# Optimization experiments

Measured on AMD Instinct MI355X. Metric: run time of the kernel, lower is better.

Reference implementation:

```python
import jax, jax.numpy as jnp
import numpy as np

HEADS = 16
DIM_HEAD = 64

def setup_inputs() -> dict:
    key = jax.random.key(0)
    ks = jax.random.split(key, 7)
    B, Nq, Dq = 4, 2048, 1024
    Nk, Dc = 1024, 768
    inner = HEADS * DIM_HEAD  # 1024
    sq = 1.0 / np.sqrt(Dq)
    sc = 1.0 / np.sqrt(Dc)
    si = 1.0 / np.sqrt(inner)
    return {
        "x": jax.random.normal(ks[0], (B, Nq, Dq), dtype=jnp.float32),
        "context": jax.random.normal(ks[1], (B, Nk, Dc), dtype=jnp.float32),
        "Wq": jax.random.normal(ks[2], (Dq, inner), dtype=jnp.float32) * sq,
        "Wk": jax.random.normal(ks[3], (Dc, inner), dtype=jnp.float32) * sc,
        "Wv": jax.random.normal(ks[4], (Dc, inner), dtype=jnp.float32) * sc,
        "Wo": jax.random.normal(ks[5], (inner, Dq), dtype=jnp.float32) * si,
        "bo": jax.random.normal(ks[6], (Dq,), dtype=jnp.float32) * 0.01,
    }

def reference(x, context, Wq, Wk, Wv, Wo, bo):
    B, Nq, _ = x.shape
    Nk = context.shape[1]
    h, dh = HEADS, DIM_HEAD
    # projections (no bias on q/k/v, matching nn.Linear(bias=False))
    q = (x @ Wq).reshape(B, Nq, h, dh)        # [B,Nq,h,dh]
    k = (context @ Wk).reshape(B, Nk, h, dh)  # [B,Nk,h,dh]
    v = (context @ Wv).reshape(B, Nk, h, dh)
    scale = 1.0 / jnp.sqrt(jnp.asarray(dh, dtype=x.dtype))
    # scores: [B,h,Nq,Nk]
    scores = jnp.einsum('bqhd,bkhd->bhqk', q, k) * scale
    attn = jax.nn.softmax(scores, axis=-1)
    out = jnp.einsum('bhqk,bkhd->bqhd', attn, v).reshape(B, Nq, h * dh)
    return out @ Wo + bo
```

## Files before the change

kernel.cpp:

```cpp
#include <hip/hip_runtime.h>

typedef __bf16 bf16;
typedef __bf16 bf16x2 __attribute__((ext_vector_type(2)));
typedef __bf16 bf16x4 __attribute__((ext_vector_type(4)));
typedef __bf16 bf16x8 __attribute__((ext_vector_type(8)));
typedef float f32x4 __attribute__((ext_vector_type(4)));

#define MFMA(a, b, c) __builtin_amdgcn_mfma_f32_16x16x32_bf16(a, b, c, 0, 0, 0)

#define GLD16(gptr, ldsptr)                                                        \
  __builtin_amdgcn_global_load_lds(                                                \
      (const __attribute__((address_space(1))) unsigned int*)(gptr),               \
      (__attribute__((address_space(3))) unsigned int*)(ldsptr), 16, 0, 0)

union I4B8 { int4 i; bf16x8 v; };
union HI { bf16x2 h; int i; };

__global__ __launch_bounds__(256) void prep_k(const float* __restrict__ x, bf16* __restrict__ xb,
                                              const float* __restrict__ ctx, bf16* __restrict__ ctxb,
                                              const float* __restrict__ Wq, bf16* __restrict__ WqT,
                                              const float* __restrict__ Wk, bf16* __restrict__ WkvT,
                                              const float* __restrict__ Wv,
                                              const float* __restrict__ Wo, bf16* __restrict__ WoT) {
  __shared__ float t[32][33];
  const int bid = blockIdx.x;
  if (bid < 5632) {
    const float* in; bf16* out; size_t i;
    if (bid < 4096) { in = x; out = xb; i = ((size_t)bid * 256 + threadIdx.x) * 8; }
    else { in = ctx; out = ctxb; i = ((size_t)(bid - 4096) * 256 + threadIdx.x) * 8; }
    const float4 a = *(const float4*)(in + i);
    const float4 b = *(const float4*)(in + i + 4);
    bf16x8 o;
    o[0] = (bf16)a.x; o[1] = (bf16)a.y; o[2] = (bf16)a.z; o[3] = (bf16)a.w;
    o[4] = (bf16)b.x; o[5] = (bf16)b.y; o[6] = (bf16)b.z; o[7] = (bf16)b.w;
    *(bf16x8*)(out + i) = o;
    return;
  }
  const int tt = bid - 5632;
  const int z = tt >> 10, rem = tt & 1023;
  const float* in; bf16* out; int R; float sc = 1.0f;
  if (z == 0)      { in = Wq; out = WqT;                R = 1024; sc = 0.18033688f; }
  else if (z == 1) { in = Wk; out = WkvT;               R = 768; }
  else if (z == 2) { in = Wv; out = WkvT + 1024 * 768;  R = 768; }
  else             { in = Wo; out = WoT;                R = 1024; }
  const int c0 = (rem & 31) * 32, r0 = (rem >> 5) * 32;
  if (r0 >= R) return;
  const int tx = threadIdx.x & 31, ty = threadIdx.x >> 5;
#pragma unroll
  for (int i = 0; i < 4; i++)
    t[ty + i * 8][tx] = in[(size_t)(r0 + ty + i * 8) * 1024 + c0 + tx];
  __syncthreads();
#pragma unroll
  for (int i = 0; i < 4; i++)
    out[(size_t)(c0 + ty + i * 8) * R + r0 + tx] = (bf16)(t[tx][ty + i * 8] * sc);
}

template <int MODE>
__device__ __forceinline__ void phase_mma(const bf16* Ls, int Abase, int Bbase,
                                          int wm, int wn, int q, int c, int swz,
                                          f32x4 (&pacc)[4][2]) {
  bf16x8 af[4][2], bb[2][2];
#pragma unroll
  for (int mi = 0; mi < 4; mi++) {
    const int rr = wm * 64 + mi * 16 + c;
#pragma unroll
    for (int kk = 0; kk < 2; kk++)
      af[mi][kk] = *(const bf16x8*)&Ls[Abase + rr * 64 + ((kk * 32 + q * 8) ^ swz)];
  }
#pragma unroll
  for (int ni = 0; ni < 2; ni++) {
    const int rn = wn * 32 + ni * 16 + c;
#pragma unroll
    for (int kk = 0; kk < 2; kk++)
      bb[ni][kk] = *(const bf16x8*)&Ls[Bbase + rn * 64 + ((kk * 32 + q * 8) ^ swz)];
  }
  __builtin_amdgcn_s_setprio(1);
#pragma unroll
  for (int mi = 0; mi < 4; mi++)
#pragma unroll
    for (int ni = 0; ni < 2; ni++)
#pragma unroll
      for (int kk = 0; kk < 2; kk++) {
        if constexpr (MODE == 2)
          pacc[mi][ni] = MFMA(af[mi][kk], bb[ni][kk], pacc[mi][ni]);
        else
          pacc[mi][ni] = MFMA(bb[ni][kk], af[mi][kk], pacc[mi][ni]);
      }
  __builtin_amdgcn_s_setprio(0);
}

template <int MODE>
__device__ __forceinline__ void gemm256(const bf16* __restrict__ A,
                                        const bf16* __restrict__ Bt,
                                        int K, int m0, int n0,
                                        void* __restrict__ C0,
                                        bf16* Ls) {
  const int tid = threadIdx.x;
  const int lane = tid & 63, w = tid >> 6;
  const int wm = w >> 2, wn = w & 3;
  const int q = lane >> 4, c = lane & 15;
  const int swz = (c & 7) * 8;

  const int rl = tid >> 3, seg = tid & 7;
  const bf16* Ag = A + (size_t)(m0 + rl) * K + ((seg ^ (rl & 7)) * 8);
  const bf16* Bg = Bt + (size_t)(n0 + rl) * K + ((seg ^ (rl & 7)) * 8);
  const size_t K64 = (size_t)K * 64, K128 = (size_t)K * 128;
  const int ws = w * 512;

  f32x4 acc[2][2][4][2] = {};

  GLD16(Ag,              &Ls[0 + ws]);
  GLD16(Ag + K64,        &Ls[4096 + ws]);
  GLD16(Ag + K128,       &Ls[8192 + ws]);
  GLD16(Ag + K128 + K64, &Ls[8192 + 4096 + ws]);
  GLD16(Bg,              &Ls[32768 + ws]);
  GLD16(Bg + K64,        &Ls[32768 + 4096 + ws]);
  GLD16(Bg + K128,       &Ls[32768 + 8192 + ws]);
  GLD16(Bg + K128 + K64, &Ls[32768 + 8192 + 4096 + ws]);

  int cur = 0;
  for (int k0 = 0; k0 < K; k0 += 64) {
    const int nxt = cur ^ 1;
    const size_t kn = (size_t)((k0 + 64 < K) ? k0 + 64 : k0);
    const int Ab = cur * 16384, Bb = 32768 + cur * 16384;
    const int An = nxt * 16384, Bn = 32768 + nxt * 16384;

    asm volatile("s_waitcnt vmcnt(2)" ::: "memory");
    asm volatile("s_barrier" ::: "memory");
    GLD16(Ag + kn,       &Ls[An + ws]);
    GLD16(Ag + kn + K64, &Ls[An + 4096 + ws]);
    phase_mma<MODE>(Ls, Ab, Bb, wm, wn, q, c, swz, acc[0][0]);

    asm volatile("s_waitcnt vmcnt(2)" ::: "memory");
    asm volatile("s_barrier" ::: "memory");
    GLD16(Ag + kn + K128,       &Ls[An + 8192 + ws]);
    GLD16(Ag + kn + K128 + K64, &Ls[An + 8192 + 4096 + ws]);
    phase_mma<MODE>(Ls, Ab, Bb + 8192, wm, wn, q, c, swz, acc[0][1]);

    asm volatile("s_barrier" ::: "memory");
    GLD16(Bg + kn,       &Ls[Bn + ws]);
    GLD16(Bg + kn + K64, &Ls[Bn + 4096 + ws]);
    phase_mma<MODE>(Ls, Ab + 8192, Bb, wm, wn, q, c, swz, acc[1][0]);

    asm volatile("s_barrier" ::: "memory");
    GLD16(Bg + kn + K128,       &Ls[Bn + 8192 + ws]);
    GLD16(Bg + kn + K128 + K64, &Ls[Bn + 8192 + 4096 + ws]);
    phase_mma<MODE>(Ls, Ab + 8192, Bb + 8192, wm, wn, q, c, swz, acc[1][1]);

    cur = nxt;
  }
  asm volatile("s_waitcnt vmcnt(0)" ::: "memory");

  if constexpr (MODE == 0) {
#pragma unroll
    for (int h = 0; h < 2; h++)
#pragma unroll
      for (int g = 0; g < 2; g++)
#pragma unroll
        for (int ni = 0; ni < 2; ni++) {
          const int col = n0 + g * 128 + wn * 32 + ni * 16 + q * 4;
#pragma unroll
          for (int mi = 0; mi < 4; mi++) {
            const int row = m0 + h * 128 + wm * 64 + mi * 16 + c;
            bf16x4 vv;
#pragma unroll
            for (int r2 = 0; r2 < 4; r2++) vv[r2] = (bf16)acc[h][g][mi][ni][r2];
            *(bf16x4*)&((bf16*)C0)[(size_t)row * 1024 + col] = vv;
          }
        }
  } else {
#pragma unroll
    for (int h = 0; h < 2; h++)
#pragma unroll
      for (int g = 0; g < 2; g++)
#pragma unroll
        for (int ni = 0; ni < 2; ni++) {
          const int col = n0 + g * 128 + wn * 32 + ni * 16 + c;
#pragma unroll
          for (int mi = 0; mi < 4; mi++) {
            const int rbase = m0 + h * 128 + wm * 64 + mi * 16 + q * 4;
            const int b = rbase >> 10, key = rbase & 1023;
            bf16* VT = (bf16*)C0;
            const int hh = col >> 6, d = col & 63;
            const int kl = key & 63;
            const int pkey = (key & ~63) | (kl & 32) | ((kl & 12) << 1) | ((kl & 16) >> 2);
            bf16x4 vv;
#pragma unroll
            for (int r2 = 0; r2 < 4; r2++) vv[r2] = (bf16)acc[h][g][mi][ni][r2];
            *(bf16x4*)&VT[((size_t)(b * 16 + hh) * 64 + d) * 1024 + pkey] = vv;
          }
        }
  }
}

__global__ __launch_bounds__(512) void proj_k(const bf16* __restrict__ xb,
                                              const bf16* __restrict__ ctxb,
                                              const bf16* __restrict__ WqT,
                                              const bf16* __restrict__ WkvT,
                                              bf16* __restrict__ Q,
                                              bf16* __restrict__ Kp,
                                              bf16* __restrict__ VT) {
  extern __shared__ __align__(16) bf16 Ls[];
  const int bid = blockIdx.x;
  if (bid < 128) {
    const int x = bid & 7, i = bid >> 3;
    const int rt = x * 4 + (i >> 2), ct = i & 3;
    gemm256<0>(xb, WqT, 1024, rt * 256, ct * 256, Q, Ls);
  } else if (bid < 192) {
    const int t = bid - 128, x = t & 7, i = t >> 3;
    const int rt = x * 2 + (i >> 2), ct = i & 3;
    gemm256<0>(ctxb, WkvT, 768, rt * 256, ct * 256, Kp, Ls);
  } else {
    const int t = bid - 192, x = t & 7, i = t >> 3;
    const int rt = x * 2 + (i >> 2), ct = i & 3;
    gemm256<2>(ctxb, WkvT + (size_t)1024 * 768, 768, rt * 256, ct * 256, VT, Ls);
  }
}

template <int MODE>
__device__ __forceinline__ void gemm_body(const bf16* __restrict__ A,
                                          const bf16* __restrict__ Bt,
                                          int K, int m0, int n0,
                                          void* __restrict__ C0,
                                          const float* __restrict__ bias,
                                          bf16* As, bf16* Bs) {
  const int tid = threadIdx.x;
  const int lane = tid & 63, wave = tid >> 6;
  const int wm = wave >> 1, wn = wave & 1;
  const int q = lane >> 4, c = lane & 15;

  f32x4 acc[4][4] = {};
  const int r = tid >> 3;
  const int col8 = ((tid & 7) * 8) ^ ((r & 7) * 8);
  const bf16* Ag = A + (size_t)(m0 + r) * K + col8;
  const bf16* Bg = Bt + (size_t)(n0 + r) * K + col8;
  const size_t K32 = (size_t)K * 32;
  bf16* AsW = As + wave * 512;
  bf16* BsW = Bs + wave * 512;
  const int swz = (c & 7) * 8;

  for (int k0 = 0; k0 < K; k0 += 64) {
    __syncthreads();
    GLD16(Ag + k0,            AsW);
    GLD16(Ag + k0 + K32,      AsW + 2048);
    GLD16(Ag + k0 + 2 * K32,  AsW + 4096);
    GLD16(Ag + k0 + 3 * K32,  AsW + 6144);
    GLD16(Bg + k0,            BsW);
    GLD16(Bg + k0 + K32,      BsW + 2048);
    GLD16(Bg + k0 + 2 * K32,  BsW + 4096);
    GLD16(Bg + k0 + 3 * K32,  BsW + 6144);
    __syncthreads();
#pragma unroll
    for (int kk = 0; kk < 2; kk++) {
      const int cx = (kk * 32 + q * 8) ^ swz;
      bf16x8 af[4], bfr[4];
#pragma unroll
      for (int mi = 0; mi < 4; mi++)
        af[mi] = *(const bf16x8*)&As[(wm * 64 + mi * 16 + c) * 64 + cx];
#pragma unroll
      for (int ni = 0; ni < 4; ni++)
        bfr[ni] = *(const bf16x8*)&Bs[(wn * 64 + ni * 16 + c) * 64 + cx];
      __builtin_amdgcn_s_setprio(1);
#pragma unroll
      for (int mi = 0; mi < 4; mi++)
#pragma unroll
        for (int ni = 0; ni < 4; ni++)
          acc[mi][ni] = MFMA(bfr[ni], af[mi], acc[mi][ni]);
      __builtin_amdgcn_s_setprio(0);
    }
  }

#pragma unroll
  for (int ni = 0; ni < 4; ni++) {
    const int col = n0 + wn * 64 + ni * 16 + q * 4;
    float4 bv4 = *(const float4*)&bias[col];
#pragma unroll
    for (int mi = 0; mi < 4; mi++) {
      const int row = m0 + wm * 64 + mi * 16 + c;
      f32x4 vv;
      vv[0] = acc[mi][ni][0] + bv4.x; vv[1] = acc[mi][ni][1] + bv4.y;
      vv[2] = acc[mi][ni][2] + bv4.z; vv[3] = acc[mi][ni][3] + bv4.w;
      *(f32x4*)&((float*)C0)[(size_t)row * 1024 + col] = vv;
    }
  }
}

__global__ __launch_bounds__(256) void out_k(const bf16* __restrict__ O,
                                             const bf16* __restrict__ WoT,
                                             float* __restrict__ out,
                                             const float* __restrict__ bo) {
  __shared__ __align__(16) bf16 As[8192];
  __shared__ __align__(16) bf16 Bs[8192];
  const int bid = blockIdx.x;
  const int s = (bid & 7) * 64 + (bid >> 3);
  gemm_body<1>(O, WoT, 1024, (s >> 3) * 128, (s & 7) * 128, out, bo, As, Bs);
}

__global__ __launch_bounds__(256, 2) void attn_k(const bf16* __restrict__ Qg,
                                                 const bf16* __restrict__ Kg,
                                                 const bf16* __restrict__ VTg,
                                                 bf16* __restrict__ Og) {
  __shared__ __align__(16) bf16 Ks[64][72];
  __shared__ __align__(16) bf16 Vt[64][72];
  const int tid = threadIdx.x;
  const int lane = tid & 63, w = tid >> 6;
  const int q = lane >> 4, c = lane & 15;
  const int bid = blockIdx.x;
  const int pair = (bid & 7) * 8 + (bid >> 6);
  const int head = pair & 15, b = pair >> 4;
  const int q0 = ((bid >> 3) & 7) * 256;

  bf16x8 aQ[4][2];
#pragma unroll
  for (int mj = 0; mj < 4; mj++)
#pragma unroll
    for (int ks = 0; ks < 2; ks++)
      aQ[mj][ks] = *(const bf16x8*)(Qg + (size_t)(b * 2048 + q0 + w * 64 + mj * 16 + c) * 1024 +
                                    head * 64 + ks * 32 + q * 8);

  f32x4 o[4][4] = {};
  f32x4 ol[4] = {};
  bf16x8 vone;
#pragma unroll
  for (int i = 0; i < 8; i++) vone[i] = (bf16)1.0f;

  const int srow = tid >> 2, sc = tid & 3;
  const bf16* Kbase = Kg + (size_t)(b * 1024 + srow) * 1024 + head * 64 + sc * 16;
  const bf16* Vbase = VTg + ((size_t)(b * 16 + head) * 64 + srow) * 1024 + sc * 16;

  bf16x8 rk0 = *(const bf16x8*)(Kbase);
  bf16x8 rk1 = *(const bf16x8*)(Kbase + 8);
  bf16x8 rv0 = *(const bf16x8*)(Vbase);
  bf16x8 rv1 = *(const bf16x8*)(Vbase + 8);

  for (int kt = 0; kt < 16; kt++) {
    __syncthreads();
    *(bf16x8*)&Ks[srow][sc * 16]     = rk0;
    *(bf16x8*)&Ks[srow][sc * 16 + 8] = rk1;
    *(bf16x8*)&Vt[srow][sc * 16]     = rv0;
    *(bf16x8*)&Vt[srow][sc * 16 + 8] = rv1;
    if (kt < 15) {
      const size_t ko = (size_t)(kt + 1) * 64 * 1024;
      const int vo = (kt + 1) * 64;
      rk0 = *(const bf16x8*)(Kbase + ko);
      rk1 = *(const bf16x8*)(Kbase + ko + 8);
      rv0 = *(const bf16x8*)(Vbase + vo);
      rv1 = *(const bf16x8*)(Vbase + vo + 8);
    }
    __syncthreads();

    f32x4 st[4][4] = {};
#pragma unroll
    for (int ks = 0; ks < 2; ks++) {
      bf16x8 ak[4];
#pragma unroll
      for (int ni = 0; ni < 4; ni++) ak[ni] = *(const bf16x8*)&Ks[ni * 16 + c][ks * 32 + q * 8];
      __builtin_amdgcn_s_setprio(1);
#pragma unroll
      for (int mj = 0; mj < 4; mj++)
#pragma unroll
        for (int ni = 0; ni < 4; ni++)
          st[mj][ni] = MFMA(ak[ni], aQ[mj][ks], st[mj][ni]);
      __builtin_amdgcn_s_setprio(0);
    }

    int pk[4][4][2];
#pragma unroll
    for (int mj = 0; mj < 4; mj++)
#pragma unroll
      for (int ni = 0; ni < 4; ni++) {
        float p0 = __builtin_amdgcn_exp2f(st[mj][ni][0]);
        float p1 = __builtin_amdgcn_exp2f(st[mj][ni][1]);
        float p2 = __builtin_amdgcn_exp2f(st[mj][ni][2]);
        float p3 = __builtin_amdgcn_exp2f(st[mj][ni][3]);
        HI h0, h1;
        h0.h[0] = (bf16)p0; h0.h[1] = (bf16)p1;
        h1.h[0] = (bf16)p2; h1.h[1] = (bf16)p3;
        pk[mj][ni][0] = h0.i;
        pk[mj][ni][1] = h1.i;
      }

#pragma unroll
    for (int ks2 = 0; ks2 < 2; ks2++) {
      bf16x8 bv[4];
#pragma unroll
      for (int ni = 0; ni < 4; ni++)
        bv[ni] = *(const bf16x8*)&Vt[ni * 16 + c][ks2 * 32 + q * 8];
#pragma unroll
      for (int mi = 0; mi < 4; mi++) {
        I4B8 pa;
        pa.i.x = pk[mi][2 * ks2][0];
        pa.i.y = pk[mi][2 * ks2][1];
        pa.i.z = pk[mi][2 * ks2 + 1][0];
        pa.i.w = pk[mi][2 * ks2 + 1][1];
        __builtin_amdgcn_s_setprio(1);
#pragma unroll
        for (int ni = 0; ni < 4; ni++)
          o[mi][ni] = MFMA(pa.v, bv[ni], o[mi][ni]);
        ol[mi] = MFMA(pa.v, vone, ol[mi]);
        __builtin_amdgcn_s_setprio(0);
      }
    }
  }

#pragma unroll
  for (int mi = 0; mi < 4; mi++) {
    float inv[4];
#pragma unroll
    for (int r = 0; r < 4; r++) inv[r] = 1.0f / ol[mi][r];
#pragma unroll
    for (int ni = 0; ni < 4; ni++)
#pragma unroll
      for (int r = 0; r < 4; r++) {
        const int qrow = q0 + w * 64 + mi * 16 + q * 4 + r;
        const int col = head * 64 + ni * 16 + c;
        Og[(size_t)(b * 2048 + qrow) * 1024 + col] = (bf16)(o[mi][ni][r] * inv[r]);
      }
  }
}

extern "C" void kernel_launch(void* const* d_in, const int* in_sizes, int n_in,
                              void* d_out, int out_size, void* d_ws, size_t ws_size,
                              hipStream_t stream) {
  (void)in_sizes; (void)n_in; (void)out_size; (void)ws_size;
  const float* x   = (const float*)d_in[0];
  const float* ctx = (const float*)d_in[1];
  const float* Wq  = (const float*)d_in[2];
  const float* Wk  = (const float*)d_in[3];
  const float* Wv  = (const float*)d_in[4];
  const float* Wo  = (const float*)d_in[5];
  const float* bo  = (const float*)d_in[6];
  float* out = (float*)d_out;

  char* ws = (char*)d_ws;
  const size_t MB = 1u << 20;
  bf16* WqT  = (bf16*)(ws);
  bf16* WkvT = (bf16*)(ws + 2 * MB);
  bf16* WoT  = (bf16*)(ws + 5 * MB);
  bf16* ctxb = (bf16*)(ws + 7 * MB);
  bf16* xb   = (bf16*)(ws + 13 * MB);
  bf16* Q    = (bf16*)(ws + 29 * MB);
  bf16* Kp   = (bf16*)(ws + 45 * MB);
  bf16* VT   = (bf16*)(ws + 53 * MB);
  bf16* O    = xb;

  prep_k<<<5632 + 4096, 256, 0, stream>>>(x, xb, ctx, ctxb, Wq, WqT, Wk, WkvT, Wv, Wo, WoT);

  proj_k<<<256, 512, 131072, stream>>>(xb, ctxb, WqT, WkvT, Q, Kp, VT);

  attn_k<<<512, 256, 0, stream>>>(Q, Kp, VT, O);

  out_k<<<512, 256, 0, stream>>>(O, WoT, out, bo);
}
```

Before: 206.3 us.

## Move output GEMM onto the pipelined 256x256 kernel and reuse register fragments

```diff
diff --git a/kernel.cpp b/kernel.cpp
--- a/kernel.cpp
+++ b/kernel.cpp
@@ -55,25 +55,29 @@
     out[(size_t)(c0 + ty + i * 8) * R + r0 + tx] = (bf16)(t[tx][ty + i * 8] * sc);
 }
 
-template <int MODE>
-__device__ __forceinline__ void phase_mma(const bf16* Ls, int Abase, int Bbase,
-                                          int wm, int wn, int q, int c, int swz,
-                                          f32x4 (&pacc)[4][2]) {
-  bf16x8 af[4][2], bb[2][2];
+__device__ __forceinline__ void ld_af(bf16x8 (&af)[4][2], const bf16* Ls, int base,
+                                      int wm, int c, int q, int swz) {
 #pragma unroll
   for (int mi = 0; mi < 4; mi++) {
     const int rr = wm * 64 + mi * 16 + c;
 #pragma unroll
     for (int kk = 0; kk < 2; kk++)
-      af[mi][kk] = *(const bf16x8*)&Ls[Abase + rr * 64 + ((kk * 32 + q * 8) ^ swz)];
-  }
+      af[mi][kk] = *(const bf16x8*)&Ls[base + rr * 64 + ((kk * 32 + q * 8) ^ swz)];
+  }
+}
+__device__ __forceinline__ void ld_bb(bf16x8 (&bb)[2][2], const bf16* Ls, int base,
+                                      int wn, int c, int q, int swz) {
 #pragma unroll
   for (int ni = 0; ni < 2; ni++) {
     const int rn = wn * 32 + ni * 16 + c;
 #pragma unroll
     for (int kk = 0; kk < 2; kk++)
-      bb[ni][kk] = *(const bf16x8*)&Ls[Bbase + rn * 64 + ((kk * 32 + q * 8) ^ swz)];
-  }
+      bb[ni][kk] = *(const bf16x8*)&Ls[base + rn * 64 + ((kk * 32 + q * 8) ^ swz)];
+  }
+}
+template <int MODE>
+__device__ __forceinline__ void mma16(f32x4 (&pacc)[4][2], const bf16x8 (&af)[4][2],
+                                      const bf16x8 (&bb)[2][2]) {
   __builtin_amdgcn_s_setprio(1);
 #pragma unroll
   for (int mi = 0; mi < 4; mi++)
@@ -94,6 +98,7 @@
                                         const bf16* __restrict__ Bt,
                                         int K, int m0, int n0,
                                         void* __restrict__ C0,
+                                        const float* __restrict__ bias,
                                         bf16* Ls) {
   const int tid = threadIdx.x;
   const int lane = tid & 63, w = tid >> 6;
@@ -112,11 +117,11 @@
   GLD16(Ag,              &Ls[0 + ws]);
   GLD16(Ag + K64,        &Ls[4096 + ws]);
   GLD16(Ag + K128,       &Ls[8192 + ws]);
-  GLD16(Ag + K128 + K64, &Ls[8192 + 4096 + ws]);
+  GLD16(Ag + K128 + K64, &Ls[12288 + ws]);
   GLD16(Bg,              &Ls[32768 + ws]);
   GLD16(Bg + K64,        &Ls[32768 + 4096 + ws]);
   GLD16(Bg + K128,       &Ls[32768 + 8192 + ws]);
-  GLD16(Bg + K128 + K64, &Ls[32768 + 8192 + 4096 + ws]);
+  GLD16(Bg + K128 + K64, &Ls[32768 + 12288 + ws]);
 
   int cur = 0;
   for (int k0 = 0; k0 < K; k0 += 64) {
@@ -125,33 +130,39 @@
     const int Ab = cur * 16384, Bb = 32768 + cur * 16384;
     const int An = nxt * 16384, Bn = 32768 + nxt * 16384;
 
+    bf16x8 af[4][2], b0[2][2], b1[2][2];
+
     asm volatile("s_waitcnt vmcnt(2)" ::: "memory");
     asm volatile("s_barrier" ::: "memory");
     GLD16(Ag + kn,       &Ls[An + ws]);
     GLD16(Ag + kn + K64, &Ls[An + 4096 + ws]);
-    phase_mma<MODE>(Ls, Ab, Bb, wm, wn, q, c, swz, acc[0][0]);
+    ld_af(af, Ls, Ab, wm, c, q, swz);
+    ld_bb(b0, Ls, Bb, wn, c, q, swz);
+    mma16<MODE>(acc[0][0], af, b0);
 
     asm volatile("s_waitcnt vmcnt(2)" ::: "memory");
     asm volatile("s_barrier" ::: "memory");
     GLD16(Ag + kn + K128,       &Ls[An + 8192 + ws]);
-    GLD16(Ag + kn + K128 + K64, &Ls[An + 8192 + 4096 + ws]);
-    phase_mma<MODE>(Ls, Ab, Bb + 8192, wm, wn, q, c, swz, acc[0][1]);
+    GLD16(Ag + kn + K128 + K64, &Ls[An + 12288 + ws]);
+    ld_bb(b1, Ls, Bb + 8192, wn, c, q, swz);
+    mma16<MODE>(acc[0][1], af, b1);
 
     asm volatile("s_barrier" ::: "memory");
     GLD16(Bg + kn,       &Ls[Bn + ws]);
     GLD16(Bg + kn + K64, &Ls[Bn + 4096 + ws]);
-    phase_mma<MODE>(Ls, Ab + 8192, Bb, wm, wn, q, c, swz, acc[1][0]);
+    ld_af(af, Ls, Ab + 8192, wm, c, q, swz);
+    mma16<MODE>(acc[1][0], af, b0);
 
     asm volatile("s_barrier" ::: "memory");
     GLD16(Bg + kn + K128,       &Ls[Bn + 8192 + ws]);
-    GLD16(Bg + kn + K128 + K64, &Ls[Bn + 8192 + 4096 + ws]);
-    phase_mma<MODE>(Ls, Ab + 8192, Bb + 8192, wm, wn, q, c, swz, acc[1][1]);
+    GLD16(Bg + kn + K128 + K64, &Ls[Bn + 12288 + ws]);
+    mma16<MODE>(acc[1][1], af, b1);
 
     cur = nxt;
   }
   asm volatile("s_waitcnt vmcnt(0)" ::: "memory");
 
-  if constexpr (MODE == 0) {
+  if constexpr (MODE == 0 || MODE == 1) {
 #pragma unroll
     for (int h = 0; h < 2; h++)
 #pragma unroll
@@ -159,13 +170,22 @@
 #pragma unroll
         for (int ni = 0; ni < 2; ni++) {
           const int col = n0 + g * 128 + wn * 32 + ni * 16 + q * 4;
+          float4 bv4 = {};
+          if constexpr (MODE == 1) bv4 = *(const float4*)&bias[col];
 #pragma unroll
           for (int mi = 0; mi < 4; mi++) {
             const int row = m0 + h * 128 + wm * 64 + mi * 16 + c;
-            bf16x4 vv;
-#pragma unroll
-            for (int r2 = 0; r2 < 4; r2++) vv[r2] = (bf16)acc[h][g][mi][ni][r2];
-            *(bf16x4*)&((bf16*)C0)[(size_t)row * 1024 + col] = vv;
+            if constexpr (MODE == 0) {
+              bf16x4 vv;
+#pragma unroll
+              for (int r2 = 0; r2 < 4; r2++) vv[r2] = (bf16)acc[h][g][mi][ni][r2];
+              *(bf16x4*)&((bf16*)C0)[(size_t)row * 1024 + col] = vv;
+            } else {
+              f32x4 vv;
+              vv[0] = acc[h][g][mi][ni][0] + bv4.x; vv[1] = acc[h][g][mi][ni][1] + bv4.y;
+              vv[2] = acc[h][g][mi][ni][2] + bv4.z; vv[3] = acc[h][g][mi][ni][3] + bv4.w;
+              *(f32x4*)&((float*)C0)[(size_t)row * 1024 + col] = vv;
+            }
           }
         }
   } else {
@@ -205,95 +225,26 @@
   if (bid < 128) {
     const int x = bid & 7, i = bid >> 3;
     const int rt = x * 4 + (i >> 2), ct = i & 3;
-    gemm256<0>(xb, WqT, 1024, rt * 256, ct * 256, Q, Ls);
+    gemm256<0>(xb, WqT, 1024, rt * 256, ct * 256, Q, nullptr, Ls);
   } else if (bid < 192) {
     const int t = bid - 128, x = t & 7, i = t >> 3;
     const int rt = x * 2 + (i >> 2), ct = i & 3;
-    gemm256<0>(ctxb, WkvT, 768, rt * 256, ct * 256, Kp, Ls);
+    gemm256<0>(ctxb, WkvT, 768, rt * 256, ct * 256, Kp, nullptr, Ls);
   } else {
     const int t = bid - 192, x = t & 7, i = t >> 3;
     const int rt = x * 2 + (i >> 2), ct = i & 3;
-    gemm256<2>(ctxb, WkvT + (size_t)1024 * 768, 768, rt * 256, ct * 256, VT, Ls);
-  }
-}
-
-template <int MODE>
-__device__ __forceinline__ void gemm_body(const bf16* __restrict__ A,
-                                          const bf16* __restrict__ Bt,
-                                          int K, int m0, int n0,
-                                          void* __restrict__ C0,
-                                          const float* __restrict__ bias,
-                                          bf16* As, bf16* Bs) {
-  const int tid = threadIdx.x;
-  const int lane = tid & 63, wave = tid >> 6;
-  const int wm = wave >> 1, wn = wave & 1;
-  const int q = lane >> 4, c = lane & 15;
-
-  f32x4 acc[4][4] = {};
-  const int r = tid >> 3;
-  const int col8 = ((tid & 7) * 8) ^ ((r & 7) * 8);
-  const bf16* Ag = A + (size_t)(m0 + r) * K + col8;
-  const bf16* Bg = Bt + (size_t)(n0 + r) * K + col8;
-  const size_t K32 = (size_t)K * 32;
-  bf16* AsW = As + wave * 512;
-  bf16* BsW = Bs + wave * 512;
-  const int swz = (c & 7) * 8;
-
-  for (int k0 = 0; k0 < K; k0 += 64) {
-    __syncthreads();
-    GLD16(Ag + k0,            AsW);
-    GLD16(Ag + k0 + K32,      AsW + 2048);
-    GLD16(Ag + k0 + 2 * K32,  AsW + 4096);
-    GLD16(Ag + k0 + 3 * K32,  AsW + 6144);
-    GLD16(Bg + k0,            BsW);
-    GLD16(Bg + k0 + K32,      BsW + 2048);
-    GLD16(Bg + k0 + 2 * K32,  BsW + 4096);
-    GLD16(Bg + k0 + 3 * K32,  BsW + 6144);
-    __syncthreads();
-#pragma unroll
-    for (int kk = 0; kk < 2; kk++) {
-      const int cx = (kk * 32 + q * 8) ^ swz;
-      bf16x8 af[4], bfr[4];
-#pragma unroll
-      for (int mi = 0; mi < 4; mi++)
-        af[mi] = *(const bf16x8*)&As[(wm * 64 + mi * 16 + c) * 64 + cx];
-#pragma unroll
-      for (int ni = 0; ni < 4; ni++)
-        bfr[ni] = *(const bf16x8*)&Bs[(wn * 64 + ni * 16 + c) * 64 + cx];
-      __builtin_amdgcn_s_setprio(1);
-#pragma unroll
-      for (int mi = 0; mi < 4; mi++)
-#pragma unroll
-        for (int ni = 0; ni < 4; ni++)
-          acc[mi][ni] = MFMA(bfr[ni], af[mi], acc[mi][ni]);
-      __builtin_amdgcn_s_setprio(0);
-    }
-  }
-
-#pragma unroll
-  for (int ni = 0; ni < 4; ni++) {
-    const int col = n0 + wn * 64 + ni * 16 + q * 4;
-    float4 bv4 = *(const float4*)&bias[col];
-#pragma unroll
-    for (int mi = 0; mi < 4; mi++) {
-      const int row = m0 + wm * 64 + mi * 16 + c;
-      f32x4 vv;
-      vv[0] = acc[mi][ni][0] + bv4.x; vv[1] = acc[mi][ni][1] + bv4.y;
-      vv[2] = acc[mi][ni][2] + bv4.z; vv[3] = acc[mi][ni][3] + bv4.w;
-      *(f32x4*)&((float*)C0)[(size_t)row * 1024 + col] = vv;
-    }
-  }
-}
-
-__global__ __launch_bounds__(256) void out_k(const bf16* __restrict__ O,
+    gemm256<2>(ctxb, WkvT + (size_t)1024 * 768, 768, rt * 256, ct * 256, VT, nullptr, Ls);
+  }
+}
+
+__global__ __launch_bounds__(512) void out_k(const bf16* __restrict__ O,
                                              const bf16* __restrict__ WoT,
                                              float* __restrict__ out,
                                              const float* __restrict__ bo) {
-  __shared__ __align__(16) bf16 As[8192];
-  __shared__ __align__(16) bf16 Bs[8192];
+  extern __shared__ __align__(16) bf16 Ls[];
   const int bid = blockIdx.x;
-  const int s = (bid & 7) * 64 + (bid >> 3);
-  gemm_body<1>(O, WoT, 1024, (s >> 3) * 128, (s & 7) * 128, out, bo, As, Bs);
+  const int s = (bid & 7) * 16 + (bid >> 3);
+  gemm256<1>(O, WoT, 1024, (s >> 2) * 256, (s & 3) * 256, out, bo, Ls);
 }
 
 __global__ __launch_bounds__(256, 2) void attn_k(const bf16* __restrict__ Qg,
@@ -450,5 +401,5 @@
 
   attn_k<<<512, 256, 0, stream>>>(Q, Kp, VT, O);
 
-  out_k<<<512, 256, 0, stream>>>(O, WoT, out, bo);
-}
+  out_k<<<128, 512, 131072, stream>>>(O, WoT, out, bo);
+}
```

New measurement: 209.0 us. No clear change (+1.4%).

## Double-buffer attention K/V tiles with XOR swizzle and reuse GEMM LDS fragments

Applied to the files above, without the earlier changes.

```diff
diff --git a/kernel.cpp b/kernel.cpp
--- a/kernel.cpp
+++ b/kernel.cpp
@@ -55,25 +55,29 @@
     out[(size_t)(c0 + ty + i * 8) * R + r0 + tx] = (bf16)(t[tx][ty + i * 8] * sc);
 }
 
-template <int MODE>
-__device__ __forceinline__ void phase_mma(const bf16* Ls, int Abase, int Bbase,
-                                          int wm, int wn, int q, int c, int swz,
-                                          f32x4 (&pacc)[4][2]) {
-  bf16x8 af[4][2], bb[2][2];
+__device__ __forceinline__ void ld_af(bf16x8 (&af)[4][2], const bf16* Ls, int base,
+                                      int wm, int c, int q, int swz) {
 #pragma unroll
   for (int mi = 0; mi < 4; mi++) {
     const int rr = wm * 64 + mi * 16 + c;
 #pragma unroll
     for (int kk = 0; kk < 2; kk++)
-      af[mi][kk] = *(const bf16x8*)&Ls[Abase + rr * 64 + ((kk * 32 + q * 8) ^ swz)];
-  }
+      af[mi][kk] = *(const bf16x8*)&Ls[base + rr * 64 + ((kk * 32 + q * 8) ^ swz)];
+  }
+}
+__device__ __forceinline__ void ld_bb(bf16x8 (&bb)[2][2], const bf16* Ls, int base,
+                                      int wn, int c, int q, int swz) {
 #pragma unroll
   for (int ni = 0; ni < 2; ni++) {
     const int rn = wn * 32 + ni * 16 + c;
 #pragma unroll
     for (int kk = 0; kk < 2; kk++)
-      bb[ni][kk] = *(const bf16x8*)&Ls[Bbase + rn * 64 + ((kk * 32 + q * 8) ^ swz)];
-  }
+      bb[ni][kk] = *(const bf16x8*)&Ls[base + rn * 64 + ((kk * 32 + q * 8) ^ swz)];
+  }
+}
+template <int MODE>
+__device__ __forceinline__ void mma16(f32x4 (&pacc)[4][2], const bf16x8 (&af)[4][2],
+                                      const bf16x8 (&bb)[2][2]) {
   __builtin_amdgcn_s_setprio(1);
 #pragma unroll
   for (int mi = 0; mi < 4; mi++)
@@ -94,6 +98,7 @@
                                         const bf16* __restrict__ Bt,
                                         int K, int m0, int n0,
                                         void* __restrict__ C0,
+                                        const float* __restrict__ bias,
                                         bf16* Ls) {
   const int tid = threadIdx.x;
   const int lane = tid & 63, w = tid >> 6;
@@ -112,11 +117,11 @@
   GLD16(Ag,              &Ls[0 + ws]);
   GLD16(Ag + K64,        &Ls[4096 + ws]);
   GLD16(Ag + K128,       &Ls[8192 + ws]);
-  GLD16(Ag + K128 + K64, &Ls[8192 + 4096 + ws]);
+  GLD16(Ag + K128 + K64, &Ls[12288 + ws]);
   GLD16(Bg,              &Ls[32768 + ws]);
   GLD16(Bg + K64,        &Ls[32768 + 4096 + ws]);
   GLD16(Bg + K128,       &Ls[32768 + 8192 + ws]);
-  GLD16(Bg + K128 + K64, &Ls[32768 + 8192 + 4096 + ws]);
+  GLD16(Bg + K128 + K64, &Ls[32768 + 12288 + ws]);
 
   int cur = 0;
   for (int k0 = 0; k0 < K; k0 += 64) {
@@ -125,33 +130,39 @@
     const int Ab = cur * 16384, Bb = 32768 + cur * 16384;
     const int An = nxt * 16384, Bn = 32768 + nxt * 16384;
 
+    bf16x8 af[4][2], b0[2][2], b1[2][2];
+
     asm volatile("s_waitcnt vmcnt(2)" ::: "memory");
     asm volatile("s_barrier" ::: "memory");
     GLD16(Ag + kn,       &Ls[An + ws]);
     GLD16(Ag + kn + K64, &Ls[An + 4096 + ws]);
-    phase_mma<MODE>(Ls, Ab, Bb, wm, wn, q, c, swz, acc[0][0]);
+    ld_af(af, Ls, Ab, wm, c, q, swz);
+    ld_bb(b0, Ls, Bb, wn, c, q, swz);
+    mma16<MODE>(acc[0][0], af, b0);
 
     asm volatile("s_waitcnt vmcnt(2)" ::: "memory");
     asm volatile("s_barrier" ::: "memory");
     GLD16(Ag + kn + K128,       &Ls[An + 8192 + ws]);
-    GLD16(Ag + kn + K128 + K64, &Ls[An + 8192 + 4096 + ws]);
-    phase_mma<MODE>(Ls, Ab, Bb + 8192, wm, wn, q, c, swz, acc[0][1]);
+    GLD16(Ag + kn + K128 + K64, &Ls[An + 12288 + ws]);
+    ld_bb(b1, Ls, Bb + 8192, wn, c, q, swz);
+    mma16<MODE>(acc[0][1], af, b1);
 
     asm volatile("s_barrier" ::: "memory");
     GLD16(Bg + kn,       &Ls[Bn + ws]);
     GLD16(Bg + kn + K64, &Ls[Bn + 4096 + ws]);
-    phase_mma<MODE>(Ls, Ab + 8192, Bb, wm, wn, q, c, swz, acc[1][0]);
+    ld_af(af, Ls, Ab + 8192, wm, c, q, swz);
+    mma16<MODE>(acc[1][0], af, b0);
 
     asm volatile("s_barrier" ::: "memory");
     GLD16(Bg + kn + K128,       &Ls[Bn + 8192 + ws]);
-    GLD16(Bg + kn + K128 + K64, &Ls[Bn + 8192 + 4096 + ws]);
-    phase_mma<MODE>(Ls, Ab + 8192, Bb + 8192, wm, wn, q, c, swz, acc[1][1]);
+    GLD16(Bg + kn + K128 + K64, &Ls[Bn + 12288 + ws]);
+    mma16<MODE>(acc[1][1], af, b1);
 
     cur = nxt;
   }
   asm volatile("s_waitcnt vmcnt(0)" ::: "memory");
 
-  if constexpr (MODE == 0) {
+  if constexpr (MODE == 0 || MODE == 1) {
 #pragma unroll
     for (int h = 0; h < 2; h++)
 #pragma unroll
@@ -159,13 +170,22 @@
 #pragma unroll
         for (int ni = 0; ni < 2; ni++) {
           const int col = n0 + g * 128 + wn * 32 + ni * 16 + q * 4;
+          float4 bv4 = {};
+          if constexpr (MODE == 1) bv4 = *(const float4*)&bias[col];
 #pragma unroll
           for (int mi = 0; mi < 4; mi++) {
             const int row = m0 + h * 128 + wm * 64 + mi * 16 + c;
-            bf16x4 vv;
-#pragma unroll
-            for (int r2 = 0; r2 < 4; r2++) vv[r2] = (bf16)acc[h][g][mi][ni][r2];
-            *(bf16x4*)&((bf16*)C0)[(size_t)row * 1024 + col] = vv;
+            if constexpr (MODE == 0) {
+              bf16x4 vv;
+#pragma unroll
+              for (int r2 = 0; r2 < 4; r2++) vv[r2] = (bf16)acc[h][g][mi][ni][r2];
+              *(bf16x4*)&((bf16*)C0)[(size_t)row * 1024 + col] = vv;
+            } else {
+              f32x4 vv;
+              vv[0] = acc[h][g][mi][ni][0] + bv4.x; vv[1] = acc[h][g][mi][ni][1] + bv4.y;
+              vv[2] = acc[h][g][mi][ni][2] + bv4.z; vv[3] = acc[h][g][mi][ni][3] + bv4.w;
+              *(f32x4*)&((float*)C0)[(size_t)row * 1024 + col] = vv;
+            }
           }
         }
   } else {
@@ -205,25 +225,24 @@
   if (bid < 128) {
     const int x = bid & 7, i = bid >> 3;
     const int rt = x * 4 + (i >> 2), ct = i & 3;
-    gemm256<0>(xb, WqT, 1024, rt * 256, ct * 256, Q, Ls);
+    gemm256<0>(xb, WqT, 1024, rt * 256, ct * 256, Q, nullptr, Ls);
   } else if (bid < 192) {
     const int t = bid - 128, x = t & 7, i = t >> 3;
     const int rt = x * 2 + (i >> 2), ct = i & 3;
-    gemm256<0>(ctxb, WkvT, 768, rt * 256, ct * 256, Kp, Ls);
+    gemm256<0>(ctxb, WkvT, 768, rt * 256, ct * 256, Kp, nullptr, Ls);
   } else {
     const int t = bid - 192, x = t & 7, i = t >> 3;
     const int rt = x * 2 + (i >> 2), ct = i & 3;
-    gemm256<2>(ctxb, WkvT + (size_t)1024 * 768, 768, rt * 256, ct * 256, VT, Ls);
-  }
-}
-
-template <int MODE>
-__device__ __forceinline__ void gemm_body(const bf16* __restrict__ A,
-                                          const bf16* __restrict__ Bt,
-                                          int K, int m0, int n0,
-                                          void* __restrict__ C0,
-                                          const float* __restrict__ bias,
-                                          bf16* As, bf16* Bs) {
+    gemm256<2>(ctxb, WkvT + (size_t)1024 * 768, 768, rt * 256, ct * 256, VT, nullptr, Ls);
+  }
+}
+
+__device__ __forceinline__ void gemm_body_out(const bf16* __restrict__ A,
+                                              const bf16* __restrict__ Bt,
+                                              int K, int m0, int n0,
+                                              float* __restrict__ C0,
+                                              const float* __restrict__ bias,
+                                              bf16* As, bf16* Bs) {
   const int tid = threadIdx.x;
   const int lane = tid & 63, wave = tid >> 6;
   const int wm = wave >> 1, wn = wave & 1;
@@ -280,7 +299,7 @@
       f32x4 vv;
       vv[0] = acc[mi][ni][0] + bv4.x; vv[1] = acc[mi][ni][1] + bv4.y;
       vv[2] = acc[mi][ni][2] + bv4.z; vv[3] = acc[mi][ni][3] + bv4.w;
-      *(f32x4*)&((float*)C0)[(size_t)row * 1024 + col] = vv;
+      *(f32x4*)&C0[(size_t)row * 1024 + col] = vv;
     }
   }
 }
@@ -293,15 +312,15 @@
   __shared__ __align__(16) bf16 Bs[8192];
   const int bid = blockIdx.x;
   const int s = (bid & 7) * 64 + (bid >> 3);
-  gemm_body<1>(O, WoT, 1024, (s >> 3) * 128, (s & 7) * 128, out, bo, As, Bs);
+  gemm_body_out(O, WoT, 1024, (s >> 3) * 128, (s & 7) * 128, out, bo, As, Bs);
 }
 
 __global__ __launch_bounds__(256, 2) void attn_k(const bf16* __restrict__ Qg,
                                                  const bf16* __restrict__ Kg,
                                                  const bf16* __restrict__ VTg,
                                                  bf16* __restrict__ Og) {
-  __shared__ __align__(16) bf16 Ks[64][72];
-  __shared__ __align__(16) bf16 Vt[64][72];
+  __shared__ __align__(16) bf16 Ks[2][64][64];
+  __shared__ __align__(16) bf16 Vt[2][64][64];
   const int tid = threadIdx.x;
   const int lane = tid & 63, w = tid >> 6;
   const int q = lane >> 4, c = lane & 15;
@@ -325,6 +344,9 @@
   for (int i = 0; i < 8; i++) vone[i] = (bf16)1.0f;
 
   const int srow = tid >> 2, sc = tid & 3;
+  const int ws0 = ((2 * sc) ^ (srow & 7)) * 8;
+  const int ws1 = ((2 * sc + 1) ^ (srow & 7)) * 8;
+  const int rsw = c & 7;
   const bf16* Kbase = Kg + (size_t)(b * 1024 + srow) * 1024 + head * 64 + sc * 16;
   const bf16* Vbase = VTg + ((size_t)(b * 16 + head) * 64 + srow) * 1024 + sc * 16;
 
@@ -332,29 +354,30 @@
   bf16x8 rk1 = *(const bf16x8*)(Kbase + 8);
   bf16x8 rv0 = *(const bf16x8*)(Vbase);
   bf16x8 rv1 = *(const bf16x8*)(Vbase + 8);
+  *(bf16x8*)&Ks[0][srow][ws0] = rk0;
+  *(bf16x8*)&Ks[0][srow][ws1] = rk1;
+  *(bf16x8*)&Vt[0][srow][ws0] = rv0;
+  *(bf16x8*)&Vt[0][srow][ws1] = rv1;
+  __syncthreads();
 
   for (int kt = 0; kt < 16; kt++) {
-    __syncthreads();
-    *(bf16x8*)&Ks[srow][sc * 16]     = rk0;
-    *(bf16x8*)&Ks[srow][sc * 16 + 8] = rk1;
-    *(bf16x8*)&Vt[srow][sc * 16]     = rv0;
-    *(bf16x8*)&Vt[srow][sc * 16 + 8] = rv1;
+    const int cur = kt & 1, nxt = cur ^ 1;
     if (kt < 15) {
-      const size_t ko = (size_t)(kt + 1) * 64 * 1024;
+      const size_t ko = (size_t)(kt + 1) * 65536;
       const int vo = (kt + 1) * 64;
       rk0 = *(const bf16x8*)(Kbase + ko);
       rk1 = *(const bf16x8*)(Kbase + ko + 8);
       rv0 = *(const bf16x8*)(Vbase + vo);
       rv1 = *(const bf16x8*)(Vbase + vo + 8);
     }
-    __syncthreads();
 
     f32x4 st[4][4] = {};
 #pragma unroll
     for (int ks = 0; ks < 2; ks++) {
       bf16x8 ak[4];
 #pragma unroll
-      for (int ni = 0; ni < 4; ni++) ak[ni] = *(const bf16x8*)&Ks[ni * 16 + c][ks * 32 + q * 8];
+      for (int ni = 0; ni < 4; ni++)
+        ak[ni] = *(const bf16x8*)&Ks[cur][ni * 16 + c][((ks * 4 + q) ^ rsw) * 8];
       __builtin_amdgcn_s_setprio(1);
 #pragma unroll
       for (int mj = 0; mj < 4; mj++)
@@ -385,7 +408,7 @@
       bf16x8 bv[4];
 #pragma unroll
       for (int ni = 0; ni < 4; ni++)
-        bv[ni] = *(const bf16x8*)&Vt[ni * 16 + c][ks2 * 32 + q * 8];
+        bv[ni] = *(const bf16x8*)&Vt[cur][ni * 16 + c][((ks2 * 4 + q) ^ rsw) * 8];
 #pragma unroll
       for (int mi = 0; mi < 4; mi++) {
         I4B8 pa;
@@ -401,6 +424,14 @@
         __builtin_amdgcn_s_setprio(0);
       }
     }
+
+    if (kt < 15) {
+      *(bf16x8*)&Ks[nxt][srow][ws0] = rk0;
+      *(bf16x8*)&Ks[nxt][srow][ws1] = rk1;
+      *(bf16x8*)&Vt[nxt][srow][ws0] = rv0;
+      *(bf16x8*)&Vt[nxt][srow][ws1] = rv1;
+    }
+    __syncthreads();
   }
 
 #pragma unroll
```

New measurement: 205.0 us. Within noise of the previous version (-0.6%).
